# Performance work log

Hardware: AMD Instinct MI355X
Metric: run time of the kernel (lower is better)

Reference implementation:

```python
import jax, jax.numpy as jnp
import numpy as np
import math

DIM = 2048
NUM_HEADS = 32
HEAD_DIM = DIM // NUM_HEADS  # 64; HEAD_DIM//2 == NUM_HEADS (required by original rope broadcasting)
SEQ_LEN = 2048
BATCH = 2
ROPE_BASE = 10000.0


def apply_rope(inputs, positions):
    # Faithful to original: positions is [L]; sinusoid broadcasts to [1, L, H/2, 1]
    # and then multiplies [B, L, N, H/2] -- the original code relies on N == H/2.
    head_dim = inputs.shape[-1]
    fraction = 2.0 * jnp.arange(head_dim // 2, dtype=inputs.dtype) / head_dim
    timescale = ROPE_BASE ** fraction                      # [H/2]
    sinusoid = positions[:, None] / timescale[None, None, :]  # [1, L, H/2]
    sinusoid = sinusoid[..., None]                         # [1, L, H/2, 1]
    sin = jnp.sin(sinusoid)
    cos = jnp.cos(sinusoid)
    first, second = jnp.split(inputs, 2, axis=-1)          # each [B, L, N, H/2]
    return jnp.concatenate([first * cos - second * sin,
                            second * cos + first * sin], axis=-1)


def setup_inputs() -> dict:
    key = jax.random.key(0)
    ks = jax.random.split(key, 9)
    s = 0.02
    inp = {
        'x': jax.random.normal(ks[0], (BATCH, SEQ_LEN, DIM), dtype=jnp.float32),
        'wq_w': jax.random.normal(ks[1], (DIM, DIM), dtype=jnp.float32) * s,
        'wq_b': jnp.zeros((DIM,), dtype=jnp.float32),
        'wk_w': jax.random.normal(ks[2], (DIM, DIM), dtype=jnp.float32) * s,
        'wk_b': jnp.zeros((DIM,), dtype=jnp.float32),
        'wv_w': jax.random.normal(ks[3], (DIM, DIM), dtype=jnp.float32) * s,
        'wv_b': jnp.zeros((DIM,), dtype=jnp.float32),
        'wo_w': jax.random.normal(ks[4], (DIM, DIM), dtype=jnp.float32) * s,
        'wo_b': jnp.zeros((DIM,), dtype=jnp.float32),
    }
    return inp


def reference(x, wq_w, wq_b, wk_w, wk_b, wv_w, wv_b, wo_w, wo_b):
    B, L, _ = x.shape
    N, H = NUM_HEADS, HEAD_DIM
    q = (x @ wq_w.T + wq_b).reshape(B, L, N, H)
    k = (x @ wk_w.T + wk_b).reshape(B, L, N, H)
    v = (x @ wv_w.T + wv_b).reshape(B, L, N, H)
    positions = jnp.arange(L, dtype=x.dtype)
    q = apply_rope(q, positions)
    k = apply_rope(k, positions)
    # [B, N, L, H]
    q = q.transpose(0, 2, 1, 3)
    k = k.transpose(0, 2, 1, 3)
    v = v.transpose(0, 2, 1, 3)
    scale = math.sqrt(H)
    scores = jnp.einsum('bnqh,bnkh->bnqk', q, k) / scale   # [B, N, L, L]
    causal = jnp.tril(jnp.ones((L, L), dtype=bool))
    scores = jnp.where(causal[None, None], scores, -jnp.inf)
    attn = jax.nn.softmax(scores, axis=-1)
    context = jnp.einsum('bnqk,bnkh->bnqh', attn, v)        # [B, N, L, H]
    context = context.transpose(0, 2, 1, 3).reshape(B, L, DIM)
    return context @ wo_w.T + wo_b
```

## Files before the change

kernel.cpp:

```cpp
#include <hip/hip_runtime.h>
#include <stdint.h>

#define D_MODEL 2048
#define SEQLEN  2048

typedef float f32x4  __attribute__((ext_vector_type(4)));
typedef float f32x16 __attribute__((ext_vector_type(16)));
typedef int   i32x4  __attribute__((ext_vector_type(4)));
typedef short s16x4  __attribute__((ext_vector_type(4)));
typedef __bf16 bf16x8 __attribute__((ext_vector_type(8)));

__device__ __forceinline__ unsigned short f2bf(float f) {
  union { float f; uint32_t u; } x; x.f = f;
  uint32_t r = (x.u + 0x7FFFu + ((x.u >> 16) & 1u)) >> 16;
  return (unsigned short)r;
}

__device__ __forceinline__ bf16x8 as_bf16x8(i32x4 v) {
  union { i32x4 i; bf16x8 b; } u; u.i = v; return u.b;
}

#define MFMA16(acc, a, b) \
  acc = __builtin_amdgcn_mfma_f32_16x16x32_bf16(as_bf16x8(a), as_bf16x8(b), acc, 0, 0, 0)
#define MFMA32(acc, a, b) \
  acc = __builtin_amdgcn_mfma_f32_32x32x16_bf16(as_bf16x8(a), as_bf16x8(b), acc, 0, 0, 0)

__device__ __forceinline__ void gload16(const void* g, void* lds) {
  __builtin_amdgcn_global_load_lds(
      (const __attribute__((address_space(1))) unsigned int*)(uintptr_t)g,
      (__attribute__((address_space(3))) unsigned int*)(uint32_t)(uintptr_t)lds,
      16, 0, 0);
}

__global__ void cvt_bf16_k(const float* __restrict__ in,
                           unsigned short* __restrict__ out, int n4) {
  int i = blockIdx.x * 256 + threadIdx.x;
  if (i < n4) {
    f32x4 v = *(const f32x4*)&in[(size_t)i * 4];
    s16x4 o;
#pragma unroll
    for (int j = 0; j < 4; ++j) o[j] = (short)f2bf(v[j]);
    *(s16x4*)&out[(size_t)i * 4] = o;
  }
}

template <int MODE>
__global__ __launch_bounds__(512) void gemm8p(
    const unsigned short* __restrict__ A,
    const unsigned short* __restrict__ W0,
    const unsigned short* __restrict__ W1,
    const unsigned short* __restrict__ W2,
    const float* __restrict__ bias0,
    const float* __restrict__ bias1,
    const float* __restrict__ bias2,
    unsigned short* __restrict__ O0,
    unsigned short* __restrict__ O1,
    unsigned short* __restrict__ O2,
    float* __restrict__ Of) {
  __shared__ alignas(16) unsigned short L[8 * 8192];

  const int t = threadIdx.x;
  const int w = t >> 6, l = t & 63;
  const int wm = w >> 2, wn = w & 3;
  const int band = l >> 4, ln = l & 15;

  const int bx = blockIdx.x;
  const int m0 = blockIdx.y * 256;

  const unsigned short* Wm;
  const float* bias;
  int nloc, mat;
  if constexpr (MODE == 0) {
    mat = bx >> 3;
    nloc = (bx & 7) * 256;
    Wm = mat == 0 ? W0 : (mat == 1 ? W1 : W2);
    bias = mat == 0 ? bias0 : (mat == 1 ? bias1 : bias2);
  } else {
    mat = 0;
    nloc = bx * 256;
    Wm = W0;
    bias = bias0;
  }

  auto stage = [&](int p, int ktile, unsigned short* buf) {
    const unsigned short* src = (p & 1) ? Wm : A;
    const int grow0 = (p & 1) ? nloc : m0;
    unsigned short* dst = buf + ((p & 1) ? 16384 : 0) + (p >> 1) * 8192;
    const int kcol = ktile * 64 + (p >> 1) * 32;
#pragma unroll
    for (int i = 0; i < 2; ++i) {
      const int pos = (w * 2 + i) * 64 + l;
      const int row = pos >> 2, blk = pos & 3;
      const int gblk = blk ^ (row & 3);
      gload16(&src[(size_t)(grow0 + row) * D_MODEL + kcol + gblk * 8],
              dst + (w * 2 + i) * 512);
    }
  };

  f32x4 acc[8][4] = {};

  stage(0, 0, L);
  stage(1, 0, L);
  stage(2, 0, L);
  stage(3, 0, L);
  asm volatile("s_waitcnt vmcnt(4)" ::: "memory");
  __builtin_amdgcn_s_barrier();

  const int arow = wm * 128;
  for (int kt = 0; kt < 32; ++kt) {
    unsigned short* Lb = L + (kt & 1) * 32768;
    unsigned short* Ln = L + ((kt & 1) ^ 1) * 32768;
    const int ktn = (kt + 1) & 31;
    i32x4 bv[4];
#pragma unroll
    for (int kh = 0; kh < 2; ++kh) {
      const unsigned short* Apl = Lb + kh * 8192;
      const unsigned short* Bpl = Lb + 16384 + kh * 8192;
#pragma unroll
      for (int hf = 0; hf < 2; ++hf) {
        i32x4 av[4];
#pragma unroll
        for (int mf = 0; mf < 4; ++mf) {
          const int row = arow + (hf * 4 + mf) * 16 + ln;
          av[mf] = *(const i32x4*)&Apl[row * 32 + ((band ^ (row & 3)) << 3)];
        }
        if (hf == 0) {
#pragma unroll
          for (int nf = 0; nf < 4; ++nf) {
            const int row = wn * 64 + nf * 16 + ln;
            bv[nf] = *(const i32x4*)&Bpl[row * 32 + ((band ^ (row & 3)) << 3)];
          }
        }
        stage(kh * 2 + hf, ktn, Ln);
        __builtin_amdgcn_s_barrier();
        asm volatile("s_waitcnt lgkmcnt(0)" ::: "memory");
        __builtin_amdgcn_sched_barrier(0);
        __builtin_amdgcn_s_setprio(1);
#pragma unroll
        for (int mf = 0; mf < 4; ++mf)
#pragma unroll
          for (int nf = 0; nf < 4; ++nf)
            MFMA16(acc[hf * 4 + mf][nf], av[mf], bv[nf]);
        __builtin_amdgcn_s_setprio(0);
        if (hf == 1) asm volatile("s_waitcnt vmcnt(4)" ::: "memory");
        __builtin_amdgcn_s_barrier();
      }
    }
  }
  asm volatile("s_waitcnt vmcnt(0)" ::: "memory");

  float bb[4];
#pragma unroll
  for (int nf = 0; nf < 4; ++nf) bb[nf] = bias[nloc + wn * 64 + nf * 16 + ln];

  if constexpr (MODE == 0) {
    unsigned short* Out = mat == 0 ? O0 : (mat == 1 ? O1 : O2);
    const bool rope = (mat < 2);
    const int head = (nloc + wn * 64) >> 6;
    const float ts = powf(10000.0f, (float)head * (1.0f / 32.0f));
#pragma unroll
    for (int am = 0; am < 8; ++am) {
#pragma unroll
      for (int r = 0; r < 4; ++r) {
        const int row = m0 + wm * 128 + am * 16 + band * 4 + r;
        float vals[4];
#pragma unroll
        for (int nf = 0; nf < 4; ++nf) vals[nf] = acc[am][nf][r] + bb[nf];
        if (rope) {
          const float pos = (float)(row & (SEQLEN - 1));
          float sv, cv;
          sincosf(pos / ts, &sv, &cv);
#pragma unroll
          for (int p = 0; p < 2; ++p) {
            const float f0 = vals[p], s0 = vals[p + 2];
            vals[p]     = f0 * cv - s0 * sv;
            vals[p + 2] = s0 * cv + f0 * sv;
          }
        }
#pragma unroll
        for (int nf = 0; nf < 4; ++nf)
          Out[(size_t)row * D_MODEL + nloc + wn * 64 + nf * 16 + ln] = f2bf(vals[nf]);
      }
    }
  } else {
#pragma unroll
    for (int am = 0; am < 8; ++am)
#pragma unroll
      for (int r = 0; r < 4; ++r) {
        const int row = m0 + wm * 128 + am * 16 + band * 4 + r;
#pragma unroll
        for (int nf = 0; nf < 4; ++nf)
          Of[(size_t)row * D_MODEL + nloc + wn * 64 + nf * 16 + ln] =
              acc[am][nf][r] + bb[nf];
      }
  }
}

__global__ __launch_bounds__(256) void attn_fwd(
    const unsigned short* __restrict__ Q, const unsigned short* __restrict__ K,
    const unsigned short* __restrict__ V, unsigned short* __restrict__ O) {
  __shared__ alignas(16) unsigned short Ks[64 * 64];
  __shared__ alignas(16) unsigned short Vt[64 * 80];

  const int t = threadIdx.x;
  const int w = t >> 6, l = t & 63;
  const int l31 = l & 31, t5 = l >> 5;
  const int bx = blockIdx.x, head = blockIdx.y, b = blockIdx.z;
  const int h0 = head * 64;
  const size_t rb = (size_t)b * SEQLEN;

  const int vg = t & 7, vrow = t >> 3;
  const int kdr = l >> 3, kdb = l & 7;

  for (int pi = 0; pi < 2; ++pi) {
    const int qt = pi ? (15 - bx) : bx;
    const int q0 = qt * 128;
    const int qg = q0 + w * 32 + l31;

    i32x4 qf[4];
#pragma unroll
    for (int hk = 0; hk < 4; ++hk)
      qf[hk] = *(const i32x4*)&Q[(rb + qg) * D_MODEL + h0 + hk * 16 + t5 * 8];

    f32x16 oacc[2] = {};
    float lsum = 0.f;

    const int nkt = qt * 2 + 2;
    for (int kt = 0; kt < nkt; ++kt) {
      const int k0 = kt * 64;
#pragma unroll
      for (int i = 0; i < 2; ++i) {
        const int drow = (i * 4 + w) * 8 + kdr;
        const int sblk = kdb ^ (drow & 7);
        gload16(&K[(rb + k0 + drow) * D_MODEL + h0 + sblk * 8], &Ks[(i * 4 + w) * 512]);
      }
#pragma unroll
      for (int i = 0; i < 2; ++i) {
        const int r = i * 32 + vrow, c8 = vg * 8;
        i32x4 vv = *(const i32x4*)&V[(rb + k0 + r) * D_MODEL + h0 + c8];
        union { i32x4 v; unsigned short s[8]; } u; u.v = vv;
#pragma unroll
        for (int j = 0; j < 8; ++j) Vt[(c8 + j) * 80 + (r ^ c8)] = u.s[j];
      }
      __syncthreads();

      f32x16 sacc[2] = {};
#pragma unroll
      for (int kvf = 0; kvf < 2; ++kvf) {
        const int krow = kvf * 32 + l31;
#pragma unroll
        for (int hk = 0; hk < 4; ++hk) {
          i32x4 a = *(const i32x4*)&Ks[krow * 64 + ((2 * hk + t5) ^ (krow & 7)) * 8];
          MFMA32(sacc[kvf], a, qf[hk]);
        }
      }

      const bool needmask = (k0 + 64 > q0 + w * 32);
      uint32_t W[2][4][2];
#pragma unroll
      for (int kvf = 0; kvf < 2; ++kvf)
#pragma unroll
        for (int g = 0; g < 4; ++g)
#pragma unroll
          for (int p = 0; p < 2; ++p) {
            uint32_t wd = 0;
#pragma unroll
            for (int e = 0; e < 2; ++e) {
              const int reg = 4 * g + 2 * p + e;
              const int kvl = kvf * 32 + 8 * g + 4 * t5 + 2 * p + e;
              float pv = __expf(sacc[kvf][reg] * 0.125f);
              if (needmask && (k0 + kvl > qg)) pv = 0.f;
              lsum += pv;
              wd |= (uint32_t)f2bf(pv) << (16 * e);
            }
            W[kvf][g][p] = wd;
          }

#pragma unroll
      for (int ks = 0; ks < 4; ++ks) {
        const int kvf = ks >> 1;
        const int gA = 2 * (ks & 1), gB = gA + 1;
        const uint32_t O0 = t5 ? W[kvf][gB][0] : W[kvf][gA][0];
        const uint32_t O1 = t5 ? W[kvf][gB][1] : W[kvf][gA][1];
        const uint32_t E0 = t5 ? W[kvf][gA][0] : W[kvf][gB][0];
        const uint32_t E1 = t5 ? W[kvf][gA][1] : W[kvf][gB][1];
        const uint32_t X0 = (uint32_t)__shfl_xor((int)E0, 32);
        const uint32_t X1 = (uint32_t)__shfl_xor((int)E1, 32);
        i32x4 pf;
        pf[0] = (int)(t5 ? X0 : O0);
        pf[1] = (int)(t5 ? X1 : O1);
        pf[2] = (int)(t5 ? O0 : X0);
        pf[3] = (int)(t5 ? O1 : X1);
#pragma unroll
        for (int hf = 0; hf < 2; ++hf) {
          const int h = hf * 32 + l31;
          i32x4 vb = *(const i32x4*)&Vt[h * 80 + ((ks * 16 + t5 * 8) ^ ((h >> 3) * 8))];
          MFMA32(oacc[hf], pf, vb);
        }
      }
      __syncthreads();
    }

    lsum += __shfl_xor(lsum, 32);
    const float inv = 1.0f / lsum;

#pragma unroll
    for (int g2 = 0; g2 < 4; ++g2)
#pragma unroll
      for (int rr = 0; rr < 4; ++rr) {
        const int rowl = rr + 8 * g2 + 4 * t5;
        const float invr = __shfl(inv, (l & 32) + rowl);
        const size_t gr = rb + q0 + w * 32 + rowl;
#pragma unroll
        for (int hf = 0; hf < 2; ++hf)
          O[gr * D_MODEL + h0 + hf * 32 + l31] = f2bf(oacc[hf][4 * g2 + rr] * invr);
      }
  }
}

extern "C" void kernel_launch(void* const* d_in, const int* in_sizes, int n_in,
                              void* d_out, int out_size, void* d_ws, size_t ws_size,
                              hipStream_t stream) {
  const float* x    = (const float*)d_in[0];
  const float* wq_w = (const float*)d_in[1];
  const float* wq_b = (const float*)d_in[2];
  const float* wk_w = (const float*)d_in[3];
  const float* wk_b = (const float*)d_in[4];
  const float* wv_w = (const float*)d_in[5];
  const float* wv_b = (const float*)d_in[6];
  const float* wo_w = (const float*)d_in[7];
  const float* wo_b = (const float*)d_in[8];
  float* out = (float*)d_out;

  unsigned short* ws  = (unsigned short*)d_ws;
  unsigned short* xb  = ws;
  unsigned short* wqb = xb  + 8388608;
  unsigned short* wkb = wqb + 4194304;
  unsigned short* wvb = wkb + 4194304;
  unsigned short* wob = wvb + 4194304;
  unsigned short* qb  = wob + 4194304;
  unsigned short* kb  = qb  + 8388608;
  unsigned short* vb  = kb  + 8388608;
  unsigned short* cb  = xb;

  cvt_bf16_k<<<8192, 256, 0, stream>>>(x, xb, 2097152);
  cvt_bf16_k<<<4096, 256, 0, stream>>>(wq_w, wqb, 1048576);
  cvt_bf16_k<<<4096, 256, 0, stream>>>(wk_w, wkb, 1048576);
  cvt_bf16_k<<<4096, 256, 0, stream>>>(wv_w, wvb, 1048576);
  cvt_bf16_k<<<4096, 256, 0, stream>>>(wo_w, wob, 1048576);

  gemm8p<0><<<dim3(24, 16), 512, 0, stream>>>(xb, wqb, wkb, wvb, wq_b, wk_b, wv_b,
                                              qb, kb, vb, nullptr);

  attn_fwd<<<dim3(8, 32, 2), 256, 0, stream>>>(qb, kb, vb, cb);

  gemm8p<1><<<dim3(8, 16), 512, 0, stream>>>(cb, wob, nullptr, nullptr, wo_b, nullptr,
                                             nullptr, nullptr, nullptr, nullptr, out);
}
```

Before: 313.7 us.

## Replace 256x256 GEMM with templated smaller-tile GEMM for more blocks

Replaces the fixed 256x256-tile, 8-wave GEMM with a templated kernel using 256x128 tiles for the QKV projection and 128x128 tiles with 4 waves for the output projection. The smaller tiles launch more blocks (768 and 512 instead of 384 and 128) so all compute units get work on the MI355X, especially for the output projection. The staging loop, LDS swizzle and pipeline are restructured into two K-half planes. The cost is less operand reuse per block and more global and LDS traffic per FLOP.

```diff
diff --git a/kernel.cpp b/kernel.cpp
--- a/kernel.cpp
+++ b/kernel.cpp
@@ -44,8 +44,8 @@
   }
 }
 
-template <int MODE>
-__global__ __launch_bounds__(512) void gemm8p(
+template <int BM, int BN, int NW, int G, int MODE>
+__global__ __launch_bounds__(NW * 64) void gemm2p(
     const unsigned short* __restrict__ A,
     const unsigned short* __restrict__ W0,
     const unsigned short* __restrict__ W1,
@@ -57,94 +57,87 @@
     unsigned short* __restrict__ O1,
     unsigned short* __restrict__ O2,
     float* __restrict__ Of) {
-  __shared__ alignas(16) unsigned short L[8 * 8192];
+  constexpr int PLANE_E = (BM + BN) * 32;
+  __shared__ alignas(16) unsigned short L[4 * PLANE_E];
 
   const int t = threadIdx.x;
   const int w = t >> 6, l = t & 63;
-  const int wm = w >> 2, wn = w & 3;
+  const int wm = w >> 1, wn = w & 1;
   const int band = l >> 4, ln = l & 15;
 
   const int bx = blockIdx.x;
-  const int m0 = blockIdx.y * 256;
+  const int m0 = blockIdx.y * BM;
 
   const unsigned short* Wm;
   const float* bias;
   int nloc, mat;
   if constexpr (MODE == 0) {
-    mat = bx >> 3;
-    nloc = (bx & 7) * 256;
+    mat = bx >> 4;
+    nloc = (bx & 15) * BN;
     Wm = mat == 0 ? W0 : (mat == 1 ? W1 : W2);
     bias = mat == 0 ? bias0 : (mat == 1 ? bias1 : bias2);
   } else {
     mat = 0;
-    nloc = bx * 256;
+    nloc = bx * BN;
     Wm = W0;
     bias = bias0;
   }
 
-  auto stage = [&](int p, int ktile, unsigned short* buf) {
-    const unsigned short* src = (p & 1) ? Wm : A;
-    const int grow0 = (p & 1) ? nloc : m0;
-    unsigned short* dst = buf + ((p & 1) ? 16384 : 0) + (p >> 1) * 8192;
-    const int kcol = ktile * 64 + (p >> 1) * 32;
-#pragma unroll
-    for (int i = 0; i < 2; ++i) {
-      const int pos = (w * 2 + i) * 64 + l;
-      const int row = pos >> 2, blk = pos & 3;
-      const int gblk = blk ^ (row & 3);
-      gload16(&src[(size_t)(grow0 + row) * D_MODEL + kcol + gblk * 8],
-              dst + (w * 2 + i) * 512);
+  auto stage = [&](int p, int ktile, int b) {
+    unsigned short* dst = L + (b * 2 + p) * PLANE_E;
+    const int kcol = ktile * 64 + p * 32;
+#pragma unroll
+    for (int i = 0; i < G; ++i) {
+      const int idx = w * G + i;
+      const int row = idx * 16 + (l >> 2);
+      const int gblk = (l & 3) ^ ((row >> 1) & 3);
+      const unsigned short* src =
+          (idx * 16 < BM) ? &A[(size_t)(m0 + row) * D_MODEL + kcol + gblk * 8]
+                          : &Wm[(size_t)(nloc + row - BM) * D_MODEL + kcol + gblk * 8];
+      gload16(src, dst + idx * 512);
     }
   };
 
-  f32x4 acc[8][4] = {};
-
-  stage(0, 0, L);
-  stage(1, 0, L);
-  stage(2, 0, L);
-  stage(3, 0, L);
-  asm volatile("s_waitcnt vmcnt(4)" ::: "memory");
+  f32x4 acc[4][4] = {};
+
+  stage(0, 0, 0);
+  stage(1, 0, 0);
+  if constexpr (G == 3) asm volatile("s_waitcnt vmcnt(3)" ::: "memory");
+  else                  asm volatile("s_waitcnt vmcnt(4)" ::: "memory");
   __builtin_amdgcn_s_barrier();
 
-  const int arow = wm * 128;
   for (int kt = 0; kt < 32; ++kt) {
-    unsigned short* Lb = L + (kt & 1) * 32768;
-    unsigned short* Ln = L + ((kt & 1) ^ 1) * 32768;
+    const int rb = kt & 1;
     const int ktn = (kt + 1) & 31;
-    i32x4 bv[4];
-#pragma unroll
-    for (int kh = 0; kh < 2; ++kh) {
-      const unsigned short* Apl = Lb + kh * 8192;
-      const unsigned short* Bpl = Lb + 16384 + kh * 8192;
-#pragma unroll
-      for (int hf = 0; hf < 2; ++hf) {
-        i32x4 av[4];
-#pragma unroll
-        for (int mf = 0; mf < 4; ++mf) {
-          const int row = arow + (hf * 4 + mf) * 16 + ln;
-          av[mf] = *(const i32x4*)&Apl[row * 32 + ((band ^ (row & 3)) << 3)];
-        }
-        if (hf == 0) {
-#pragma unroll
-          for (int nf = 0; nf < 4; ++nf) {
-            const int row = wn * 64 + nf * 16 + ln;
-            bv[nf] = *(const i32x4*)&Bpl[row * 32 + ((band ^ (row & 3)) << 3)];
-          }
-        }
-        stage(kh * 2 + hf, ktn, Ln);
-        __builtin_amdgcn_s_barrier();
-        asm volatile("s_waitcnt lgkmcnt(0)" ::: "memory");
-        __builtin_amdgcn_sched_barrier(0);
-        __builtin_amdgcn_s_setprio(1);
-#pragma unroll
-        for (int mf = 0; mf < 4; ++mf)
-#pragma unroll
-          for (int nf = 0; nf < 4; ++nf)
-            MFMA16(acc[hf * 4 + mf][nf], av[mf], bv[nf]);
-        __builtin_amdgcn_s_setprio(0);
-        if (hf == 1) asm volatile("s_waitcnt vmcnt(4)" ::: "memory");
-        __builtin_amdgcn_s_barrier();
-      }
+#pragma unroll
+    for (int p = 0; p < 2; ++p) {
+      const unsigned short* Apl = L + (rb * 2 + p) * PLANE_E;
+      const unsigned short* Bpl = Apl + BM * 32;
+      i32x4 av[4], bv[4];
+#pragma unroll
+      for (int mf = 0; mf < 4; ++mf) {
+        const int row = wm * 64 + mf * 16 + ln;
+        av[mf] = *(const i32x4*)&Apl[row * 32 + (((band ^ (row >> 1)) & 3) << 3)];
+      }
+#pragma unroll
+      for (int nf = 0; nf < 4; ++nf) {
+        const int row = wn * 64 + nf * 16 + ln;
+        bv[nf] = *(const i32x4*)&Bpl[row * 32 + (((band ^ (row >> 1)) & 3) << 3)];
+      }
+      stage(p, ktn, rb ^ 1);
+      __builtin_amdgcn_s_barrier();
+      asm volatile("s_waitcnt lgkmcnt(0)" ::: "memory");
+      __builtin_amdgcn_sched_barrier(0);
+      __builtin_amdgcn_s_setprio(1);
+#pragma unroll
+      for (int mf = 0; mf < 4; ++mf)
+#pragma unroll
+        for (int nf = 0; nf < 4; ++nf)
+          MFMA16(acc[mf][nf], av[mf], bv[nf]);
+      __builtin_amdgcn_s_setprio(0);
+      if constexpr (G == 3) asm volatile("s_waitcnt vmcnt(3)" ::: "memory");
+      else                  asm volatile("s_waitcnt vmcnt(4)" ::: "memory");
+      __builtin_amdgcn_s_barrier();
     }
   }
   asm volatile("s_waitcnt vmcnt(0)" ::: "memory");
@@ -159,22 +152,22 @@
     const int head = (nloc + wn * 64) >> 6;
     const float ts = powf(10000.0f, (float)head * (1.0f / 32.0f));
 #pragma unroll
-    for (int am = 0; am < 8; ++am) {
+    for (int mf = 0; mf < 4; ++mf) {
 #pragma unroll
       for (int r = 0; r < 4; ++r) {
-        const int row = m0 + wm * 128 + am * 16 + band * 4 + r;
+        const int row = m0 + wm * 64 + mf * 16 + band * 4 + r;
         float vals[4];
 #pragma unroll
-        for (int nf = 0; nf < 4; ++nf) vals[nf] = acc[am][nf][r] + bb[nf];
+        for (int nf = 0; nf < 4; ++nf) vals[nf] = acc[mf][nf][r] + bb[nf];
         if (rope) {
           const float pos = (float)(row & (SEQLEN - 1));
           float sv, cv;
           sincosf(pos / ts, &sv, &cv);
 #pragma unroll
-          for (int p = 0; p < 2; ++p) {
-            const float f0 = vals[p], s0 = vals[p + 2];
-            vals[p]     = f0 * cv - s0 * sv;
-            vals[p + 2] = s0 * cv + f0 * sv;
+          for (int pp = 0; pp < 2; ++pp) {
+            const float f0 = vals[pp], s0 = vals[pp + 2];
+            vals[pp]     = f0 * cv - s0 * sv;
+            vals[pp + 2] = s0 * cv + f0 * sv;
           }
         }
 #pragma unroll
@@ -184,14 +177,14 @@
     }
   } else {
 #pragma unroll
-    for (int am = 0; am < 8; ++am)
+    for (int mf = 0; mf < 4; ++mf)
 #pragma unroll
       for (int r = 0; r < 4; ++r) {
-        const int row = m0 + wm * 128 + am * 16 + band * 4 + r;
+        const int row = m0 + wm * 64 + mf * 16 + band * 4 + r;
 #pragma unroll
         for (int nf = 0; nf < 4; ++nf)
           Of[(size_t)row * D_MODEL + nloc + wn * 64 + nf * 16 + ln] =
-              acc[am][nf][r] + bb[nf];
+              acc[mf][nf][r] + bb[nf];
       }
   }
 }
@@ -349,11 +342,12 @@
   cvt_bf16_k<<<4096, 256, 0, stream>>>(wv_w, wvb, 1048576);
   cvt_bf16_k<<<4096, 256, 0, stream>>>(wo_w, wob, 1048576);
 
-  gemm8p<0><<<dim3(24, 16), 512, 0, stream>>>(xb, wqb, wkb, wvb, wq_b, wk_b, wv_b,
-                                              qb, kb, vb, nullptr);
+  gemm2p<256, 128, 8, 3, 0><<<dim3(48, 16), 512, 0, stream>>>(
+      xb, wqb, wkb, wvb, wq_b, wk_b, wv_b, qb, kb, vb, nullptr);
 
   attn_fwd<<<dim3(8, 32, 2), 256, 0, stream>>>(qb, kb, vb, cb);
 
-  gemm8p<1><<<dim3(8, 16), 512, 0, stream>>>(cb, wob, nullptr, nullptr, wo_b, nullptr,
-                                             nullptr, nullptr, nullptr, nullptr, out);
-}
+  gemm2p<128, 128, 4, 4, 1><<<dim3(16, 32), 256, 0, stream>>>(
+      cb, wob, nullptr, nullptr, wo_b, nullptr, nullptr,
+      nullptr, nullptr, nullptr, out);
+}
```

New measurement: 283.8 us. 1.11x faster.
